# Optimization experiments

Hardware: AMD Instinct MI355X
Metric: run time of the kernel (lower is better)

## Reference

```python
import jax, jax.numpy as jnp
import numpy as np

N, E, D_IN, D_H, D_OUT, L = 100000, 300000, 128, 128, 3, 12


def _gconv(x, edges, W0, b0, W1, b1):
    # pytorch3d GraphConv: w0(x) + gather_scatter(w1(x), edges)
    y = x @ W0.T + b0                      # [N, D_out] self transform
    n = x @ W1.T + b1                      # [N, D_out] neighbor transform
    # undirected: each edge (i, j) adds n[j] to out[i] and n[i] to out[j]
    agg = jnp.zeros_like(y)
    agg = agg.at[edges[:, 0]].add(n[edges[:, 1]])
    agg = agg.at[edges[:, 1]].add(n[edges[:, 0]])
    return y + agg


def setup_inputs() -> dict:
    key = jax.random.key(0)
    ks = jax.random.split(key, 20)

    def lin(k, out_d, in_d):
        s = 1.0 / np.sqrt(in_d)
        return jax.random.uniform(k, (out_d, in_d), jnp.float32, -s, s)

    def bias(k, out_d, in_d):
        s = 1.0 / np.sqrt(in_d)
        return jax.random.uniform(k, (out_d,), jnp.float32, -s, s)

    features = jax.random.normal(ks[0], (N, D_IN), jnp.float32)
    edges = jax.random.randint(ks[1], (E, 2), 0, N, dtype=jnp.int32)

    # first layer (in -> hidden)
    W0_1, b0_1 = lin(ks[2], D_H, D_IN), bias(ks[3], D_H, D_IN)
    W1_1, b1_1 = lin(ks[4], D_H, D_IN), bias(ks[5], D_H, D_IN)
    # 12 hidden layers (hidden -> hidden), stacked for lax.scan
    W0_h = jax.vmap(lambda k: lin(k, D_H, D_H))(jax.random.split(ks[6], L))
    b0_h = jax.vmap(lambda k: bias(k, D_H, D_H))(jax.random.split(ks[7], L))
    W1_h = jax.vmap(lambda k: lin(k, D_H, D_H))(jax.random.split(ks[8], L))
    b1_h = jax.vmap(lambda k: bias(k, D_H, D_H))(jax.random.split(ks[9], L))
    # last layer (hidden -> out)
    W0_l, b0_l = lin(ks[10], D_OUT, D_H), bias(ks[11], D_OUT, D_H)
    W1_l, b1_l = lin(ks[12], D_OUT, D_H), bias(ks[13], D_OUT, D_H)

    return {
        "features": features, "edges": edges,
        "W0_1": W0_1, "b0_1": b0_1, "W1_1": W1_1, "b1_1": b1_1,
        "W0_h": W0_h, "b0_h": b0_h, "W1_h": W1_h, "b1_h": b1_h,
        "W0_l": W0_l, "b0_l": b0_l, "W1_l": W1_l, "b1_l": b1_l,
    }


def reference(features, edges, W0_1, b0_1, W1_1, b1_1,
              W0_h, b0_h, W1_h, b1_h, W0_l, b0_l, W1_l, b1_l):
    x = jax.nn.relu(_gconv(features, edges, W0_1, b0_1, W1_1, b1_1))
    residual = x

    def step(x, p):
        W0, b0, W1, b1 = p
        return jax.nn.relu(_gconv(x, edges, W0, b0, W1, b1)), None

    x, _ = jax.lax.scan(step, x, (W0_h, b0_h, W1_h, b1_h))
    auxiliary = x
    vertices = _gconv(residual + x, edges, W0_l, b0_l, W1_l, b1_l)
    return vertices, auxiliary
```

## Files before the change

### kernel.cpp

```cpp
#include <hip/hip_runtime.h>
#include <hip/hip_bf16.h>

#define D 128
#define OSTR 136
#define CHUNK 12544

typedef float f32x4  __attribute__((ext_vector_type(4)));
typedef unsigned int u32x4 __attribute__((ext_vector_type(4)));
typedef __attribute__((ext_vector_type(8))) __bf16 bh8;

union UV { uint4 u; bh8 h; };

__device__ inline float bf2f(unsigned short u) {
    union { unsigned int i; float f; } x; x.i = ((unsigned int)u) << 16; return x.f;
}
__device__ inline unsigned short f2bf(float f) {
    union { float f; unsigned int i; } x; x.f = f;
    return (unsigned short)((x.i + 0x7fffu + ((x.i >> 16) & 1u)) >> 16);
}
__device__ inline void acc2(unsigned int u, float& a, float& b) {
    union { unsigned int i; float f; } lo, hi;
    lo.i = u << 16; hi.i = u & 0xffff0000u;
    a += lo.f; b += hi.f;
}
__device__ inline unsigned int addb2(unsigned int ua, unsigned int ub) {
    union { unsigned int i; float f; } la, ha, lb, hb;
    la.i = ua << 16; ha.i = ua & 0xffff0000u;
    lb.i = ub << 16; hb.i = ub & 0xffff0000u;
    return ((unsigned int)f2bf(ha.f + hb.f) << 16) | f2bf(la.f + lb.f);
}

__global__ void k_hist(const int* __restrict__ edges, int E, int* __restrict__ deg) {
    int e = blockIdx.x * blockDim.x + threadIdx.x;
    if (e < E) {
        atomicAdd(&deg[edges[2 * e]], 1);
        atomicAdd(&deg[edges[2 * e + 1]], 1);
    }
}

__global__ void k_scan1(const int* __restrict__ deg, int n,
                        int* __restrict__ incl, int* __restrict__ bsum) {
    __shared__ int lds[1024];
    int t = threadIdx.x;
    int i = blockIdx.x * 1024 + t;
    int v = (i < n) ? deg[i] : 0;
    int cur = v;
    lds[t] = cur;
    __syncthreads();
    for (int off = 1; off < 1024; off <<= 1) {
        int add = (t >= off) ? lds[t - off] : 0;
        __syncthreads();
        cur += add;
        lds[t] = cur;
        __syncthreads();
    }
    if (i < n) incl[i] = cur;
    if (t == 1023) bsum[blockIdx.x] = cur;
}

__global__ void k_scan2(int* __restrict__ bsum, int nb) {
    __shared__ int lds[128];
    int t = threadIdx.x;
    int v = (t < nb) ? bsum[t] : 0;
    int cur = v;
    lds[t] = cur;
    __syncthreads();
    for (int off = 1; off < 128; off <<= 1) {
        int add = (t >= off) ? lds[t - off] : 0;
        __syncthreads();
        cur += add;
        lds[t] = cur;
        __syncthreads();
    }
    if (t < nb) bsum[t] = cur - v;
}

__global__ void k_scan3(const int* __restrict__ incl, const int* __restrict__ deg,
                        const int* __restrict__ bsum, int n, int twoE,
                        int* __restrict__ rowstart, int* __restrict__ cursor) {
    int i = blockIdx.x * blockDim.x + threadIdx.x;
    if (i < n) {
        int r = incl[i] - deg[i] + bsum[i >> 10];
        rowstart[i] = r;
        cursor[i] = r;
    }
    if (i == 0) rowstart[n] = twoE;
}

__global__ void k_fill(const int* __restrict__ edges, int E,
                       int* __restrict__ cursor, int* __restrict__ adj) {
    int e = blockIdx.x * blockDim.x + threadIdx.x;
    if (e < E) {
        int a = edges[2 * e], b = edges[2 * e + 1];
        adj[atomicAdd(&cursor[a], 1)] = b;
        adj[atomicAdd(&cursor[b], 1)] = a;
    }
}

__global__ void k_wprep(const float* __restrict__ W0_1, const float* __restrict__ W1_1,
                        const float* __restrict__ W0_h, const float* __restrict__ W1_h,
                        unsigned short* __restrict__ wb) {
    int idx = blockIdx.x * 256 + threadIdx.x;
    if (idx >= 13 * 2 * 128 * 128) return;
    int k = idx & 127;
    int o = (idx >> 7) & 127;
    int m = (idx >> 14) & 1;
    int l = idx >> 15;
    const float* src = (l == 0) ? (m ? W1_1 : W0_1)
                                : ((m ? W1_h : W0_h) + (size_t)(l - 1) * 16384);
    float v = src[o * 128 + k];
    int kk = m * 128 + k;
    wb[(size_t)l * 32768 + (kk >> 5) * 4096 + o * 32 + (kk & 31)] = f2bf(v);
}

__global__ void k_cvt(const float* __restrict__ in, unsigned short* __restrict__ out, int n4) {
    int i = blockIdx.x * blockDim.x + threadIdx.x;
    if (i >= n4) return;
    f32x4 v = *(const f32x4*)&in[(size_t)i * 4];
    unsigned short u[4];
    #pragma unroll
    for (int j = 0; j < 4; ++j) u[j] = f2bf(v[j]);
    *(uint2*)&out[(size_t)i * 4] = *(uint2*)u;
}

__global__ __launch_bounds__(256) void k_agg(
    const unsigned short* __restrict__ x, const int* __restrict__ rowstart,
    const int* __restrict__ adj, unsigned short* __restrict__ s, int n) {
    int node = (blockIdx.x & 7) * CHUNK + (blockIdx.x >> 3) * 4 + (threadIdx.x >> 6);
    int lane = threadIdx.x & 63;
    if (node >= n) return;
    int r0 = rowstart[node], r1 = rowstart[node + 1];
    float a[8], b[8];
    #pragma unroll
    for (int k = 0; k < 8; ++k) { a[k] = 0.f; b[k] = 0.f; }
    for (int p = r0; p < r1; p += 8) {
        int q = p + (lane & 7);
        int idx = (q < r1) ? adj[q] : 0;
        unsigned int u[8];
        #pragma unroll
        for (int k = 0; k < 8; ++k) {
            int j = __shfl(idx, k);
            u[k] = *(const unsigned int*)&x[(size_t)j * D + lane * 2];
        }
        #pragma unroll
        for (int k = 0; k < 8; ++k)
            if (p + k < r1) acc2(u[k], a[k], b[k]);
    }
    float f0 = ((a[0] + a[1]) + (a[2] + a[3])) + ((a[4] + a[5]) + (a[6] + a[7]));
    float f1 = ((b[0] + b[1]) + (b[2] + b[3])) + ((b[4] + b[5]) + (b[6] + b[7]));
    unsigned int out = ((unsigned int)f2bf(f1) << 16) | f2bf(f0);
    *(unsigned int*)&s[(size_t)node * D + lane * 2] = out;
}

__global__ __launch_bounds__(256) void k_gemm(
    const unsigned short* __restrict__ x,
    const unsigned short* __restrict__ s,
    const unsigned short* __restrict__ wb,
    const float* __restrict__ b0, const float* __restrict__ b1,
    const int* __restrict__ deg,
    unsigned short* __restrict__ out,
    float* __restrict__ out32,
    const unsigned short* __restrict__ resid,
    unsigned short* __restrict__ zout,
    int n, int do_relu) {
    __shared__ __align__(16) unsigned short LDS[64 * OSTR];
    int node0 = (blockIdx.x & 7) * CHUNK + (blockIdx.x >> 3) * 64;
    if (node0 >= n) return;
    int t = threadIdx.x;
    int lane = t & 63;
    int wave = t >> 6;
    int wm = (wave >> 1) * 32;
    int wn = (wave & 1) * 64;
    int mlane = lane & 15;
    int quad = lane >> 4;

    f32x4 acc[2][4];
    #pragma unroll
    for (int i = 0; i < 2; ++i)
        #pragma unroll
        for (int j = 0; j < 4; ++j) acc[i][j] = (f32x4){0.f, 0.f, 0.f, 0.f};

    #pragma unroll
    for (int kc = 0; kc < 8; ++kc) {
        const unsigned short* srcA = (kc < 4) ? x : s;
        int kbase = (kc & 3) * 32;
        bh8 af[2], bf_[4];
        #pragma unroll
        for (int i = 0; i < 2; ++i) {
            int g = node0 + wm + i * 16 + mlane;
            UV v; v.u = (uint4){0u, 0u, 0u, 0u};
            if (g < n) v.u = *(const uint4*)&srcA[(size_t)g * D + kbase + quad * 8];
            af[i] = v.h;
        }
        #pragma unroll
        for (int j = 0; j < 4; ++j)
            bf_[j] = *(const bh8*)&wb[(size_t)kc * 4096 + (wn + j * 16 + mlane) * 32 + quad * 8];
        #pragma unroll
        for (int i = 0; i < 2; ++i)
            #pragma unroll
            for (int j = 0; j < 4; ++j)
                acc[i][j] = __builtin_amdgcn_mfma_f32_16x16x32_bf16(af[i], bf_[j], acc[i][j], 0, 0, 0);
    }

    #pragma unroll
    for (int i = 0; i < 2; ++i) {
        int mrow = wm + i * 16 + quad * 4;
        #pragma unroll
        for (int j = 0; j < 4; ++j) {
            int nn = wn + j * 16 + mlane;
            float b0v = b0[nn], b1v = b1[nn];
            #pragma unroll
            for (int r = 0; r < 4; ++r) {
                int g = node0 + mrow + r;
                float dg = (g < n) ? (float)deg[g] : 0.f;
                float val = acc[i][j][r] + b0v + dg * b1v;
                if (do_relu) val = fmaxf(val, 0.f);
                LDS[(mrow + r) * OSTR + nn] = f2bf(val);
            }
        }
    }
    __syncthreads();
    #pragma unroll
    for (int pass = 0; pass < 4; ++pass) {
        int row = pass * 16 + (t >> 4);
        int seg = (t & 15) * 8;
        int g = node0 + row;
        if (g < n) {
            u32x4 v = *(const u32x4*)&LDS[row * OSTR + seg];
            __builtin_nontemporal_store(v, (u32x4*)&out[(size_t)g * D + seg]);
            if (zout) {
                u32x4 rr = *(const u32x4*)&resid[(size_t)g * D + seg];
                u32x4 zz;
                zz.x = addb2(v.x, rr.x);
                zz.y = addb2(v.y, rr.y);
                zz.z = addb2(v.z, rr.z);
                zz.w = addb2(v.w, rr.w);
                __builtin_nontemporal_store(zz, (u32x4*)&zout[(size_t)g * D + seg]);
            }
        }
    }
    if (out32) {
        #pragma unroll
        for (int pass = 0; pass < 8; ++pass) {
            int row = pass * 8 + (t >> 5);
            int seg = (t & 31) * 4;
            int g = node0 + row;
            if (g < n) {
                f32x4 v;
                #pragma unroll
                for (int j = 0; j < 4; ++j) v[j] = bf2f(LDS[row * OSTR + seg + j]);
                __builtin_nontemporal_store(v, (f32x4*)&out32[(size_t)g * D + seg]);
            }
        }
    }
}

__global__ void k_last(const unsigned short* __restrict__ z, const unsigned short* __restrict__ sz,
                       const float* __restrict__ W0, const float* __restrict__ b0,
                       const float* __restrict__ W1, const float* __restrict__ b1,
                       const int* __restrict__ deg, float* __restrict__ vert, int n) {
    int t = threadIdx.x;
    int lane = t & 63;
    int node = blockIdx.x * 4 + (t >> 6);
    if (node >= n) return;
    float z0 = bf2f(z[(size_t)node * D + lane]), z1 = bf2f(z[(size_t)node * D + 64 + lane]);
    float s0 = bf2f(sz[(size_t)node * D + lane]), s1 = bf2f(sz[(size_t)node * D + 64 + lane]);
    float dg = (float)deg[node];
    #pragma unroll
    for (int o = 0; o < 3; ++o) {
        float p = z0 * W0[o * D + lane] + z1 * W0[o * D + 64 + lane]
                + s0 * W1[o * D + lane] + s1 * W1[o * D + 64 + lane];
        for (int off = 32; off > 0; off >>= 1) p += __shfl_down(p, off);
        if (lane == 0) vert[(size_t)node * 3 + o] = p + b0[o] + dg * b1[o];
    }
}

extern "C" void kernel_launch(void* const* d_in, const int* in_sizes, int n_in,
                              void* d_out, int out_size, void* d_ws, size_t ws_size,
                              hipStream_t stream) {
    const float* features = (const float*)d_in[0];
    const int*   edges    = (const int*)d_in[1];
    const float* W0_1 = (const float*)d_in[2];
    const float* b0_1 = (const float*)d_in[3];
    const float* W1_1 = (const float*)d_in[4];
    const float* b1_1 = (const float*)d_in[5];
    const float* W0_h = (const float*)d_in[6];
    const float* b0_h = (const float*)d_in[7];
    const float* W1_h = (const float*)d_in[8];
    const float* b1_h = (const float*)d_in[9];
    const float* W0_l = (const float*)d_in[10];
    const float* b0_l = (const float*)d_in[11];
    const float* W1_l = (const float*)d_in[12];
    const float* b1_l = (const float*)d_in[13];

    const int N_ = 100000, E_ = 300000;
    float* vert = (float*)d_out;
    float* aux  = (float*)d_out + (size_t)N_ * 3;

    char* w = (char*)d_ws;
    auto alloc = [&](size_t bytes) {
        char* p = w;
        w += (bytes + 255) & ~(size_t)255;
        return p;
    };
    unsigned short* wb    = (unsigned short*)alloc((size_t)13 * 32768 * 2);
    unsigned short* xf    = (unsigned short*)alloc((size_t)N_ * D * 2);
    unsigned short* resid = (unsigned short*)alloc((size_t)N_ * D * 2);
    unsigned short* xa    = (unsigned short*)alloc((size_t)N_ * D * 2);
    unsigned short* xb    = (unsigned short*)alloc((size_t)N_ * D * 2);
    unsigned short* sb    = (unsigned short*)alloc((size_t)N_ * D * 2);
    int* deg    = (int*)alloc((size_t)N_ * 4);
    int* incl   = (int*)alloc((size_t)N_ * 4);
    int* rowst  = (int*)alloc((size_t)(N_ + 1) * 4);
    int* cursor = (int*)alloc((size_t)N_ * 4);
    int* bsum   = (int*)alloc(128 * 4);
    int* adj    = (int*)alloc((size_t)2 * E_ * 4);

    hipMemsetAsync(deg, 0, (size_t)N_ * 4, stream);
    k_hist<<<(E_ + 255) / 256, 256, 0, stream>>>(edges, E_, deg);
    int nb = (N_ + 1023) / 1024;
    k_scan1<<<nb, 1024, 0, stream>>>(deg, N_, incl, bsum);
    k_scan2<<<1, 128, 0, stream>>>(bsum, nb);
    k_scan3<<<(N_ + 255) / 256, 256, 0, stream>>>(incl, deg, bsum, N_, 2 * E_, rowst, cursor);
    k_fill<<<(E_ + 255) / 256, 256, 0, stream>>>(edges, E_, cursor, adj);

    k_wprep<<<(13 * 2 * 16384 + 255) / 256, 256, 0, stream>>>(W0_1, W1_1, W0_h, W1_h, wb);
    k_cvt<<<(N_ * D / 4 + 255) / 256, 256, 0, stream>>>(features, xf, N_ * D / 4);

    int gblocks = 8 * ((CHUNK) / 64);
    int ablocks = 8 * ((CHUNK) / 4);
    int ablocks_plain = (N_ + 3) / 4;

    k_agg<<<ablocks, 256, 0, stream>>>(xf, rowst, adj, sb, N_);
    k_gemm<<<gblocks, 256, 0, stream>>>(xf, sb, wb, b0_1, b1_1, deg, resid,
                                        nullptr, nullptr, nullptr, N_, 1);

    for (int h = 0; h < 12; ++h) {
        const unsigned short* in = (h == 0) ? resid : ((h & 1) ? xa : xb);
        unsigned short* outp = (h & 1) ? xb : xa;
        float* o32 = (h == 11) ? aux : nullptr;
        const unsigned short* radd = (h == 11) ? resid : nullptr;
        unsigned short* zo = (h == 11) ? xf : nullptr;
        k_agg<<<ablocks, 256, 0, stream>>>(in, rowst, adj, sb, N_);
        k_gemm<<<gblocks, 256, 0, stream>>>(in, sb, wb + (size_t)(1 + h) * 32768,
                                            b0_h + h * 128, b1_h + h * 128, deg,
                                            outp, o32, radd, zo, N_, 1);
    }

    k_agg<<<ablocks, 256, 0, stream>>>(xf, rowst, adj, sb, N_);
    k_last<<<ablocks_plain, 256, 0, stream>>>(xf, sb, W0_l, b0_l, W1_l, b1_l, deg, vert, N_);
}
```

Measured before the change: 1.271 ms.

## Fuse final aggregation with output projection, double-buffer GEMM loads, nontemporal gathers

The final k_agg and k_last kernels are merged into one kernel that gathers neighbour features and applies the 3-output projection in registers, so the aggregated buffer is never written out and read back. The GEMM K-loop now prefetches the next chunk's A and B fragments into a second register set while the MFMAs on the current chunk run. Neighbour gathers use nontemporal loads to reduce cache pollution. The trade-offs are higher register pressure in the GEMM, and gathered rows that repeat across nodes may lose cache reuse.

```diff
diff --git a/kernel.cpp b/kernel.cpp
--- a/kernel.cpp
+++ b/kernel.cpp
@@ -140,7 +140,8 @@
         #pragma unroll
         for (int k = 0; k < 8; ++k) {
             int j = __shfl(idx, k);
-            u[k] = *(const unsigned int*)&x[(size_t)j * D + lane * 2];
+            u[k] = __builtin_nontemporal_load(
+                (const unsigned int*)&x[(size_t)j * D + lane * 2]);
         }
         #pragma unroll
         for (int k = 0; k < 8; ++k)
@@ -180,26 +181,36 @@
         #pragma unroll
         for (int j = 0; j < 4; ++j) acc[i][j] = (f32x4){0.f, 0.f, 0.f, 0.f};
 
-    #pragma unroll
-    for (int kc = 0; kc < 8; ++kc) {
+    uint4 ra[2][2];
+    bh8 rb[2][4];
+    auto LDK = [&](int kc, int st) {
         const unsigned short* srcA = (kc < 4) ? x : s;
         int kbase = (kc & 3) * 32;
-        bh8 af[2], bf_[4];
         #pragma unroll
         for (int i = 0; i < 2; ++i) {
             int g = node0 + wm + i * 16 + mlane;
-            UV v; v.u = (uint4){0u, 0u, 0u, 0u};
-            if (g < n) v.u = *(const uint4*)&srcA[(size_t)g * D + kbase + quad * 8];
-            af[i] = v.h;
+            uint4 v = {0u, 0u, 0u, 0u};
+            if (g < n) v = *(const uint4*)&srcA[(size_t)g * D + kbase + quad * 8];
+            ra[st][i] = v;
         }
         #pragma unroll
         for (int j = 0; j < 4; ++j)
-            bf_[j] = *(const bh8*)&wb[(size_t)kc * 4096 + (wn + j * 16 + mlane) * 32 + quad * 8];
-        #pragma unroll
-        for (int i = 0; i < 2; ++i)
-            #pragma unroll
-            for (int j = 0; j < 4; ++j)
-                acc[i][j] = __builtin_amdgcn_mfma_f32_16x16x32_bf16(af[i], bf_[j], acc[i][j], 0, 0, 0);
+            rb[st][j] = *(const bh8*)&wb[(size_t)kc * 4096 + (wn + j * 16 + mlane) * 32 + quad * 8];
+    };
+
+    LDK(0, 0);
+    #pragma unroll
+    for (int kc = 0; kc < 8; ++kc) {
+        int cs = kc & 1;
+        if (kc < 7) LDK(kc + 1, cs ^ 1);
+        bh8 a0, a1;
+        { UV v; v.u = ra[cs][0]; a0 = v.h; }
+        { UV v; v.u = ra[cs][1]; a1 = v.h; }
+        #pragma unroll
+        for (int j = 0; j < 4; ++j) {
+            acc[0][j] = __builtin_amdgcn_mfma_f32_16x16x32_bf16(a0, rb[cs][j], acc[0][j], 0, 0, 0);
+            acc[1][j] = __builtin_amdgcn_mfma_f32_16x16x32_bf16(a1, rb[cs][j], acc[1][j], 0, 0, 0);
+        }
     }
 
     #pragma unroll
@@ -255,21 +266,44 @@
     }
 }
 
-__global__ void k_last(const unsigned short* __restrict__ z, const unsigned short* __restrict__ sz,
-                       const float* __restrict__ W0, const float* __restrict__ b0,
-                       const float* __restrict__ W1, const float* __restrict__ b1,
-                       const int* __restrict__ deg, float* __restrict__ vert, int n) {
-    int t = threadIdx.x;
-    int lane = t & 63;
-    int node = blockIdx.x * 4 + (t >> 6);
+__global__ __launch_bounds__(256) void k_lastagg(
+    const unsigned short* __restrict__ z, const int* __restrict__ rowstart,
+    const int* __restrict__ adj,
+    const float* __restrict__ W0, const float* __restrict__ b0,
+    const float* __restrict__ W1, const float* __restrict__ b1,
+    float* __restrict__ vert, int n) {
+    int node = blockIdx.x * 4 + (threadIdx.x >> 6);
+    int lane = threadIdx.x & 63;
     if (node >= n) return;
-    float z0 = bf2f(z[(size_t)node * D + lane]), z1 = bf2f(z[(size_t)node * D + 64 + lane]);
-    float s0 = bf2f(sz[(size_t)node * D + lane]), s1 = bf2f(sz[(size_t)node * D + 64 + lane]);
-    float dg = (float)deg[node];
+    int r0 = rowstart[node], r1 = rowstart[node + 1];
+    float a[8], b[8];
+    #pragma unroll
+    for (int k = 0; k < 8; ++k) { a[k] = 0.f; b[k] = 0.f; }
+    for (int p = r0; p < r1; p += 8) {
+        int q = p + (lane & 7);
+        int idx = (q < r1) ? adj[q] : 0;
+        unsigned int u[8];
+        #pragma unroll
+        for (int k = 0; k < 8; ++k) {
+            int j = __shfl(idx, k);
+            u[k] = __builtin_nontemporal_load(
+                (const unsigned int*)&z[(size_t)j * D + lane * 2]);
+        }
+        #pragma unroll
+        for (int k = 0; k < 8; ++k)
+            if (p + k < r1) acc2(u[k], a[k], b[k]);
+    }
+    float f0 = ((a[0] + a[1]) + (a[2] + a[3])) + ((a[4] + a[5]) + (a[6] + a[7]));
+    float f1 = ((b[0] + b[1]) + (b[2] + b[3])) + ((b[4] + b[5]) + (b[6] + b[7]));
+    unsigned int zz = *(const unsigned int*)&z[(size_t)node * D + lane * 2];
+    float z0, z1;
+    { union { unsigned int i; float f; } lo, hi;
+      lo.i = zz << 16; hi.i = zz & 0xffff0000u; z0 = lo.f; z1 = hi.f; }
+    float dg = (float)(r1 - r0);
     #pragma unroll
     for (int o = 0; o < 3; ++o) {
-        float p = z0 * W0[o * D + lane] + z1 * W0[o * D + 64 + lane]
-                + s0 * W1[o * D + lane] + s1 * W1[o * D + 64 + lane];
+        float p = z0 * W0[o * D + 2 * lane] + z1 * W0[o * D + 2 * lane + 1]
+                + f0 * W1[o * D + 2 * lane] + f1 * W1[o * D + 2 * lane + 1];
         for (int off = 32; off > 0; off >>= 1) p += __shfl_down(p, off);
         if (lane == 0) vert[(size_t)node * 3 + o] = p + b0[o] + dg * b1[o];
     }
@@ -329,7 +363,7 @@
 
     int gblocks = 8 * ((CHUNK) / 64);
     int ablocks = 8 * ((CHUNK) / 4);
-    int ablocks_plain = (N_ + 3) / 4;
+    int lblocks = (N_ + 3) / 4;
 
     k_agg<<<ablocks, 256, 0, stream>>>(xf, rowst, adj, sb, N_);
     k_gemm<<<gblocks, 256, 0, stream>>>(xf, sb, wb, b0_1, b1_1, deg, resid,
@@ -347,6 +381,6 @@
                                             outp, o32, radd, zo, N_, 1);
     }
 
-    k_agg<<<ablocks, 256, 0, stream>>>(xf, rowst, adj, sb, N_);
-    k_last<<<ablocks_plain, 256, 0, stream>>>(xf, sb, W0_l, b0_l, W1_l, b1_l, deg, vert, N_);
-}
+    k_lastagg<<<lblocks, 256, 0, stream>>>(xf, rowst, adj, W0_l, b0_l, W1_l, b1_l,
+                                           vert, N_);
+}
```

New measurement: 1.479 ms. 16.3% more time.
